# Kernel optimization log

Measured on AMD Instinct MI355X. Metric: run time of the kernel, lower is better.

## Reference

```python
import jax, jax.numpy as jnp
import numpy as np

MAX_SESSIONS = 400
P_A = 0.5
EF_FLOOR = 1.3
OUT_MIN = 15.0 / (24.0 * 60.0)


def _sm2(p):
    # p: [B, MAX_SESSIONS] float
    f = p.dtype
    B = p.shape[0]
    I0 = jnp.ones((B,), f)          # interval state; I_i stays 1.0 (never mutated in torch)
    n0 = jnp.zeros((B,), f)         # repetition count
    EF0 = jnp.full((B,), 2.5, f)    # easiness factor

    def step(carry, p_i):
        I, n, EF = carry
        q = p_i * 5.0
        correct = (q >= 3.0).astype(f)
        brk = (p_i == -1.0).astype(f)
        n_is_0 = (n == 0.0).astype(f)
        n_is_1 = (n == 1.0).astype(f)
        n_is_2p = (n >= 2.0).astype(f)
        # I_i == 1.0 always, so I_i*mask -> mask, I_i*6*mask -> 6*mask
        I_n = I * EF * n_is_2p + n_is_0 + 6.0 * n_is_1
        I_n = I_n * correct + (1.0 - correct)
        I = I_n * (1.0 - brk) + I * brk
        I = jnp.clip(I, 1.0, 274.0)
        # EF update is unconditional in the original (even on break / incorrect)
        EF = EF + (0.1 - (5.0 - q) * (0.08 + (5.0 - q) * 0.02))
        EF = jnp.maximum(EF, EF_FLOOR)
        n = (n + 1.0) * correct + n * (1.0 - correct)
        return (I, n, EF), None

    (I, n, EF), _ = jax.lax.scan(step, (I0, n0, EF0), p.T)  # scan over time axis
    h_t = I / P_A
    return jnp.clip(h_t, OUT_MIN, 274.0)


def setup_inputs() -> dict:
    key = jax.random.key(0)
    B = 524288
    p = jax.random.uniform(key, (B, MAX_SESSIONS), dtype=jnp.float32)
    return {"p": p}


def reference(p):
    return _sm2(p)
```

## Files before the change

kernel.cpp:

```cpp
#include <hip/hip_runtime.h>

#define TSTEPS 400
#define ROWS   256

constexpr float OUT_MIN = 15.0f / (24.0f * 60.0f);

__device__ __forceinline__ void sm2_step(float p_i, float& I, float& n, float& EF) {
    float q = p_i * 5.0f;
    bool correct = (q >= 3.0f);
    float I_n = (n == 0.0f) ? 1.0f : ((n == 1.0f) ? 6.0f : I * EF);
    I_n = correct ? I_n : 1.0f;
    I = fminf(fmaxf(I_n, 1.0f), 274.0f);
    float d = 5.0f - q;
    EF = EF + (0.1f - d * (0.08f + d * 0.02f));
    EF = fmaxf(EF, 1.3f);
    n = correct ? (n + 1.0f) : n;
}

__device__ __forceinline__ void scan4(const float4 v, float& I, float& n, float& EF) {
    sm2_step(v.x, I, n, EF);
    sm2_step(v.y, I, n, EF);
    sm2_step(v.z, I, n, EF);
    sm2_step(v.w, I, n, EF);
}

__global__ __launch_bounds__(256, 4) void sm2_kernel(const float* __restrict__ p,
                                                     float* __restrict__ out) {
    const int t = threadIdx.x;
    const size_t row = (size_t)blockIdx.x * ROWS + t;
    const float* __restrict__ src = p + row * (size_t)TSTEPS;

    float I = 1.0f, n = 0.0f, EF = 2.5f;

    float4 A[8], B[8];

    #pragma unroll
    for (int j = 0; j < 8; ++j)
        A[j] = *reinterpret_cast<const float4*>(src + j * 4);

    #pragma unroll 1
    for (int k = 0; k < 5; ++k) {
        const float* __restrict__ sB = src + (size_t)(2 * k + 1) * 32;
        #pragma unroll
        for (int j = 0; j < 8; ++j)
            B[j] = *reinterpret_cast<const float4*>(sB + j * 4);
        #pragma unroll
        for (int j = 0; j < 8; ++j) scan4(A[j], I, n, EF);

        const float* __restrict__ sA = src + (size_t)(2 * k + 2) * 32;
        #pragma unroll
        for (int j = 0; j < 8; ++j)
            A[j] = *reinterpret_cast<const float4*>(sA + j * 4);
        #pragma unroll
        for (int j = 0; j < 8; ++j) scan4(B[j], I, n, EF);
    }

    {
        const float* __restrict__ sB = src + 11 * 32;
        #pragma unroll
        for (int j = 0; j < 8; ++j)
            B[j] = *reinterpret_cast<const float4*>(sB + j * 4);
        #pragma unroll
        for (int j = 0; j < 8; ++j) scan4(A[j], I, n, EF);

        const float* __restrict__ sT = src + 384;
        #pragma unroll
        for (int j = 0; j < 4; ++j)
            A[j] = *reinterpret_cast<const float4*>(sT + j * 4);
        #pragma unroll
        for (int j = 0; j < 8; ++j) scan4(B[j], I, n, EF);
        #pragma unroll
        for (int j = 0; j < 4; ++j) scan4(A[j], I, n, EF);
    }

    float h = I * 2.0f;
    out[row] = fminf(fmaxf(h, OUT_MIN), 274.0f);
}

extern "C" void kernel_launch(void* const* d_in, const int* in_sizes, int n_in,
                              void* d_out, int out_size, void* d_ws, size_t ws_size,
                              hipStream_t stream) {
    const float* p = (const float*)d_in[0];
    float* out = (float*)d_out;
    int B = out_size;
    int blocks = B / ROWS;
    sm2_kernel<<<blocks, ROWS, 0, stream>>>(p, out);
}
```

Measured before the change: 1.046 ms.

## Stage per-row chunks through LDS with async global_load_lds double buffering

Replaces the strided per-thread float4 loads, where each lane reads its own 1600-byte row, with wave-cooperative global_load_lds transfers. Eight lanes now cover one row's 128-byte chunk, which makes the global accesses coalesced. Data is double-buffered in LDS with an XOR swizzle to avoid bank conflicts, and manual vmcnt/lgkmcnt waits overlap the next chunk's load with the scan. Occupancy drops to 2 blocks per CU because of the 64KB LDS tile, and the hand-written waitcnt sequencing is fragile.

```diff
diff --git a/kernel.cpp b/kernel.cpp
--- a/kernel.cpp
+++ b/kernel.cpp
@@ -2,6 +2,7 @@
 
 #define TSTEPS 400
 #define ROWS   256
+#define WAVES  4
 
 constexpr float OUT_MIN = 15.0f / (24.0f * 60.0f);
 
@@ -24,54 +25,77 @@
     sm2_step(v.w, I, n, EF);
 }
 
-__global__ __launch_bounds__(256, 4) void sm2_kernel(const float* __restrict__ p,
+__device__ __forceinline__ void gload_lds16(const float* g, float4* lds) {
+    __builtin_amdgcn_global_load_lds(
+        (const __attribute__((address_space(1))) unsigned int*)g,
+        (__attribute__((address_space(3))) unsigned int*)lds, 16, 0, 0);
+}
+
+__global__ __launch_bounds__(256, 2) void sm2_kernel(const float* __restrict__ p,
                                                      float* __restrict__ out) {
+    __shared__ float4 tile[2][WAVES][64][8];
+
     const int t = threadIdx.x;
+    const int w = t >> 6;
+    const int l = t & 63;
     const size_t row = (size_t)blockIdx.x * ROWS + t;
-    const float* __restrict__ src = p + row * (size_t)TSTEPS;
+
+    const int rl0  = l >> 3;
+    const int gsrc = (l & 7) ^ rl0;
+    const float* gbase = p + ((size_t)blockIdx.x * ROWS + (size_t)w * 64 + rl0) * TSTEPS
+                           + (size_t)gsrc * 4;
 
     float I = 1.0f, n = 0.0f, EF = 2.5f;
 
-    float4 A[8], B[8];
+#define STAGE(BUF, CH)                                                          \
+    do {                                                                        \
+        const int _off = ((CH) == 12) ? 368 : (CH) * 32;                        \
+        _Pragma("unroll")                                                       \
+        for (int _i = 0; _i < 8; ++_i)                                          \
+            gload_lds16(gbase + (size_t)_i * 8 * TSTEPS + _off,                 \
+                        &tile[BUF][w][_i * 8][0]);                              \
+    } while (0)
 
-    #pragma unroll
-    for (int j = 0; j < 8; ++j)
-        A[j] = *reinterpret_cast<const float4*>(src + j * 4);
+    STAGE(0, 0);
+    STAGE(1, 1);
+
+    const int key = l & 7;
 
     #pragma unroll 1
-    for (int k = 0; k < 5; ++k) {
-        const float* __restrict__ sB = src + (size_t)(2 * k + 1) * 32;
+    for (int ch = 0; ch <= 10; ++ch) {
+        asm volatile("s_waitcnt vmcnt(8)" ::: "memory");
+        __builtin_amdgcn_sched_barrier(0);
+        const int buf = ch & 1;
+        float4 v[8];
         #pragma unroll
-        for (int j = 0; j < 8; ++j)
-            B[j] = *reinterpret_cast<const float4*>(sB + j * 4);
+        for (int g = 0; g < 8; ++g) v[g] = tile[buf][w][l][g ^ key];
+        asm volatile("s_waitcnt lgkmcnt(0)" ::: "memory");
+        __builtin_amdgcn_sched_barrier(0);
+        STAGE(buf, ch + 2);
         #pragma unroll
-        for (int j = 0; j < 8; ++j) scan4(A[j], I, n, EF);
-
-        const float* __restrict__ sA = src + (size_t)(2 * k + 2) * 32;
-        #pragma unroll
-        for (int j = 0; j < 8; ++j)
-            A[j] = *reinterpret_cast<const float4*>(sA + j * 4);
-        #pragma unroll
-        for (int j = 0; j < 8; ++j) scan4(B[j], I, n, EF);
+        for (int g = 0; g < 8; ++g) scan4(v[g], I, n, EF);
     }
 
     {
-        const float* __restrict__ sB = src + 11 * 32;
+        asm volatile("s_waitcnt vmcnt(8)" ::: "memory");
+        __builtin_amdgcn_sched_barrier(0);
+        float4 v[8];
         #pragma unroll
-        for (int j = 0; j < 8; ++j)
-            B[j] = *reinterpret_cast<const float4*>(sB + j * 4);
+        for (int g = 0; g < 8; ++g) v[g] = tile[1][w][l][g ^ key];
         #pragma unroll
-        for (int j = 0; j < 8; ++j) scan4(A[j], I, n, EF);
+        for (int g = 0; g < 8; ++g) scan4(v[g], I, n, EF);
+    }
 
-        const float* __restrict__ sT = src + 384;
+    {
+        asm volatile("s_waitcnt vmcnt(0)" ::: "memory");
+        __builtin_amdgcn_sched_barrier(0);
+        float4 v[4];
         #pragma unroll
-        for (int j = 0; j < 4; ++j)
-            A[j] = *reinterpret_cast<const float4*>(sT + j * 4);
+        for (int g = 4; g < 8; ++g) v[g - 4] = tile[0][w][l][g ^ key];
         #pragma unroll
-        for (int j = 0; j < 8; ++j) scan4(B[j], I, n, EF);
-        #pragma unroll
-        for (int j = 0; j < 4; ++j) scan4(A[j], I, n, EF);
+        for (int g = 0; g < 4; ++g) scan4(v[g], I, n, EF);
     }
+#undef STAGE
 
     float h = I * 2.0f;
     out[row] = fminf(fmaxf(h, OUT_MIN), 274.0f);
```

Measured after the change: 1.040 ms. No clear change (-0.6%).
